# Kernel tuning notes

Measured on AMD Instinct MI355X. Metric: run time of the kernel, lower is better.

Reference implementation:

```python
import jax, jax.numpy as jnp
import numpy as np

CUTOFF = 5.0
MASK_VALUE = -1
N_POINTS = 1024
MAX_NEIGHBOURS = 128
_CELL = np.diag([20.0, 20.0, 20.0]).astype(np.float32)


def _cell_grid():
    # mirrors get_cell_list: integer image multiples bounding the cutoff sphere
    vol = abs(float(np.dot(_CELL[0], np.cross(_CELL[1], _CELL[2]))))
    maxes = []
    for v in range(3):
        clen = float(np.linalg.norm(np.cross(_CELL[(v + 1) % 3], _CELL[(v + 2) % 3])))
        maxes.append(int(np.ceil(CUTOFF / vol * clen)))
    g = np.array(np.meshgrid(np.arange(-maxes[0], maxes[0] + 1),
                             np.arange(-maxes[1], maxes[1] + 1),
                             np.arange(-maxes[2], maxes[2] + 1)))
    reshaped = g.T.reshape(-1, 3)  # (G, 3) integer cell shifts, G = 27 here
    return reshaped.astype(np.int32), reshaped.astype(np.float32) @ _CELL


def setup_inputs() -> dict:
    key = jax.random.key(0)
    cell_list, grid_points = _cell_grid()
    positions = jax.random.uniform(key, (N_POINTS, 3), dtype=jnp.float32, minval=0.0, maxval=20.0)
    return {
        'positions': positions,
        'grid_points': jnp.asarray(grid_points),
        'cell_list': jnp.asarray(cell_list),
        'max_neighbours': MAX_NEIGHBOURS,
    }


def reference(positions, grid_points, cell_list, max_neighbours):
    # Faithful translation of PeriodicBoundary.get_neighbours (include_self=False, include_images=True)
    n = positions.shape[0]
    # all periodic image copies of every point: (G*n, 3)
    neighbours = (grid_points[:, None, :] + positions[None, :, :]).reshape(-1, 3)
    # squared distances from every centre to every image point: (n, G*n)
    d2 = jnp.sum((neighbours[None, :, :] - positions[:, None, :]) ** 2, axis=-1)
    neigh_mask = d2 < CUTOFF * CUTOFF
    # exclude self-interaction (index j == i within the home cell block)
    self_mask = jnp.arange(neighbours.shape[0])[None, :] == jnp.arange(n, dtype=jnp.int32)[:, None]
    neigh_mask = neigh_mask & ~self_mask
    # per-row argwhere compaction into fixed-size padded neighbour lists
    to_idx = jax.vmap(lambda m: jnp.argwhere(m, size=max_neighbours, fill_value=MASK_VALUE))(neigh_mask)[..., 0]
    # cell shift for each flat image index: cells[j] = cell_list[j // n]
    cells = jnp.repeat(cell_list, n, axis=0)  # (G*n, 3)
    cell_indices = jax.vmap(jnp.take, (None, 0, None))(cells, to_idx, 0)  # (n, M, 3)
    neigh = jnp.where(to_idx == MASK_VALUE, MASK_VALUE, to_idx % n)  # (n, M)
    actual_max = jnp.max(neigh_mask.sum(axis=1))
    return neigh, cell_indices, actual_max
```

## Files before the change

kernel.cpp:

```cpp
#include <hip/hip_runtime.h>


#define NPTS 1024
#define MAXN 128
#define CUT2 25.0f
#define NTHR 512
#define NWAVE (NTHR / 64)
#define MAXCHUNK (NPTS / 64)

template <int NC>
__global__ __launch_bounds__(NTHR) void pb_fused(
    const float* __restrict__ positions,
    const float* __restrict__ grid_points,
    const int*   __restrict__ cell_list,
    int n, int G_rt,
    int* __restrict__ neigh,
    int* __restrict__ cells_out,
    int* __restrict__ actual_max)
{
    const int G = (NC > 0) ? NC : G_rt;
    const int nchunk = (n + 63) >> 6;

    __shared__ float4 sp[NPTS];
    __shared__ float4 sgrid[32];
    __shared__ int    scell[32][3];
    __shared__ unsigned long long smask[32][MAXCHUNK];
    __shared__ int    s_choff[32][MAXCHUNK];
    __shared__ int    s_cnt[32];
    __shared__ int    s_coff[32];
    __shared__ int    s_total;

    const int tid = threadIdx.x;

    {
        float* spf = (float*)sp;
        const int n3 = n * 3;
        for (int j = tid; j < n3; j += NTHR) {
            const int p = j / 3, c = j - 3 * p;
            spf[4 * p + c] = positions[j];
        }
        if (tid < G) {
            sgrid[tid] = make_float4(grid_points[3 * tid + 0],
                                     grid_points[3 * tid + 1],
                                     grid_points[3 * tid + 2], 0.0f);
            scell[tid][0] = cell_list[3 * tid + 0];
            scell[tid][1] = cell_list[3 * tid + 1];
            scell[tid][2] = cell_list[3 * tid + 2];
        }
        unsigned long long* smf = (unsigned long long*)smask;
        for (int t = tid; t < G * MAXCHUNK; t += NTHR) smf[t] = 0ull;
    }
    __syncthreads();

    const int i    = blockIdx.x;
    const int wid  = tid >> 6;
    const int lane = tid & 63;

    const float4 ci = sp[i];
    const float cx = ci.x, cy = ci.y, cz = ci.z;

    unsigned long long svmask;
    {
        const float4 g4 = sgrid[lane < G ? lane : 0];
        bool sv = false;
        if (lane < G) {
            const float bx = fmaxf(fmaxf(g4.x - cx, cx - (g4.x + 20.0f)), 0.0f);
            const float by = fmaxf(fmaxf(g4.y - cy, cy - (g4.y + 20.0f)), 0.0f);
            const float bz = fmaxf(fmaxf(g4.z - cz, cz - (g4.z + 20.0f)), 0.0f);
            sv = (bx * bx + by * by + bz * bz < CUT2 + 1.0e-3f);
        }
        svmask = __ballot(sv);
    }

    for (unsigned long long m = svmask; m; m &= m - 1ull) {
        const int c = (int)__builtin_ctzll(m);
        const float4 g4 = sgrid[c];
        for (int ch = wid; ch < nchunk; ch += NWAVE) {
            const int p = (ch << 6) + lane;
            const float4 q = sp[p < n ? p : 0];
            float d2;
            {
#pragma clang fp contract(off)
                const float ex = (g4.x + q.x) - cx;
                const float ey = (g4.y + q.y) - cy;
                const float ez = (g4.z + q.z) - cz;
                d2 = (ex * ex + ey * ey) + ez * ez;
            }
            const bool pred = (p < n) && (d2 < CUT2) && (c * n + p != i);
            const unsigned long long mm = __ballot(pred);
            if (lane == 0) smask[c][ch] = mm;
        }
    }
    __syncthreads();

    if (tid < G * MAXCHUNK) {
        const int c = tid >> 4, ch = tid & 15;
        const int cnt = (ch < nchunk) ? (int)__popcll(smask[c][ch]) : 0;
        int inc = cnt;
#pragma unroll
        for (int d = 1; d < 16; d <<= 1) {
            const int v = __shfl_up(inc, d, 16);
            if ((lane & 15) >= d) inc += v;
        }
        s_choff[c][ch] = inc - cnt;
        if (ch == 15) s_cnt[c] = inc;
    }
    __syncthreads();

    if (wid == 0) {
        const int x = (lane < G) ? s_cnt[lane] : 0;
        int inc = x;
#pragma unroll
        for (int d = 1; d < 32; d <<= 1) {
            const int v = __shfl_up(inc, d, 64);
            if (lane >= d) inc += v;
        }
        if (lane < G) s_coff[lane] = inc - x;
        if (lane == G - 1) s_total = inc;
    }
    __syncthreads();

    int* __restrict__ nrow = neigh + (size_t)i * MAXN;
    int* __restrict__ crow = cells_out + (size_t)i * MAXN * 3;

    {
        const unsigned long long lmask = (1ull << lane) - 1ull;
        for (unsigned long long m = svmask; m; m &= m - 1ull) {
            const int c = (int)__builtin_ctzll(m);
            const int offc = s_coff[c];
            if (offc >= MAXN) continue;
            const int c0 = scell[c][0], c1 = scell[c][1], c2 = scell[c][2];
            for (int ch = wid; ch < nchunk; ch += NWAVE) {
                const unsigned long long mm = smask[c][ch];
                if (!mm) continue;
                const int base2 = offc + s_choff[c][ch];
                if (base2 >= MAXN) continue;
                const int before = __popcll(mm & lmask);
                const int idx = base2 + before;
                if (((mm >> lane) & 1ull) && idx < MAXN) {
                    nrow[idx] = (ch << 6) + lane;
                    crow[3 * idx + 0] = c0;
                    crow[3 * idx + 1] = c1;
                    crow[3 * idx + 2] = c2;
                }
            }
        }
    }

    const int total = s_total;
    const int f0 = scell[G - 1][0], f1 = scell[G - 1][1], f2 = scell[G - 1][2];
    const int base = total < MAXN ? total : MAXN;
    for (int kk = base + tid; kk < MAXN; kk += NTHR) {
        nrow[kk] = -1;
        crow[3 * kk + 0] = f0;
        crow[3 * kk + 1] = f1;
        crow[3 * kk + 2] = f2;
    }

    if (tid == 0) atomicMax(actual_max, total);
}

extern "C" void kernel_launch(void* const* d_in, const int* in_sizes, int n_in,
                              void* d_out, int out_size, void* d_ws, size_t ws_size,
                              hipStream_t stream) {
    const float* positions   = (const float*)d_in[0];
    const float* grid_points = (const float*)d_in[1];
    const int*   cell_list   = (const int*)d_in[2];

    const int n = in_sizes[0] / 3;
    const int G = in_sizes[1] / 3;

    int* out        = (int*)d_out;
    int* neigh      = out;
    int* cells_out  = out + (size_t)n * MAXN;
    int* actual_max = out + (size_t)n * MAXN * 4;

    if (G == 27 && G * MAXCHUNK <= NTHR)
        pb_fused<27><<<n, NTHR, 0, stream>>>(positions, grid_points, cell_list,
                                             n, G, neigh, cells_out, actual_max);
    else
        pb_fused<0><<<n, NTHR, 0, stream>>>(positions, grid_points, cell_list,
                                            n, G, neigh, cells_out, actual_max);
}
```

Measured before the change: 21.02 us.

## Stage neighbour rows in LDS and write out with coalesced int4 stores

Each block now writes its compacted neighbour indices, cell shifts and padding into a shared-memory row buffer, then copies that buffer to global memory with contiguous 16-byte stores from the first 128 threads. This replaces scattered 4-byte global writes whose addresses follow the per-chunk compaction order. The position load into shared memory is also changed to read float4 vectors before de-interleaving. The cost is an extra 2 KB of LDS and one more block-wide barrier before the output copy.

```diff
diff --git a/kernel.cpp b/kernel.cpp
--- a/kernel.cpp
+++ b/kernel.cpp
@@ -29,13 +29,30 @@
     __shared__ int    s_cnt[32];
     __shared__ int    s_coff[32];
     __shared__ int    s_total;
+    __shared__ int4   srow4[MAXN];
+
+    int* srow = (int*)srow4;
 
     const int tid = threadIdx.x;
 
     {
         float* spf = (float*)sp;
         const int n3 = n * 3;
-        for (int j = tid; j < n3; j += NTHR) {
+        const int n4 = n3 >> 2;
+        const float4* pos4 = (const float4*)positions;
+        for (int t = tid; t < n4; t += NTHR) {
+            const float4 f = pos4[t];
+            const int j = 4 * t;
+            const int j0 = j,     p0 = j0 / 3, c0 = j0 - 3 * p0;
+            const int j1 = j + 1, p1 = j1 / 3, c1 = j1 - 3 * p1;
+            const int j2 = j + 2, p2 = j2 / 3, c2 = j2 - 3 * p2;
+            const int j3 = j + 3, p3 = j3 / 3, c3 = j3 - 3 * p3;
+            spf[4 * p0 + c0] = f.x;
+            spf[4 * p1 + c1] = f.y;
+            spf[4 * p2 + c2] = f.z;
+            spf[4 * p3 + c3] = f.w;
+        }
+        for (int j = (n4 << 2) + tid; j < n3; j += NTHR) {
             const int p = j / 3, c = j - 3 * p;
             spf[4 * p + c] = positions[j];
         }
@@ -120,9 +137,6 @@
     }
     __syncthreads();
 
-    int* __restrict__ nrow = neigh + (size_t)i * MAXN;
-    int* __restrict__ crow = cells_out + (size_t)i * MAXN * 3;
-
     {
         const unsigned long long lmask = (1ull << lane) - 1ull;
         for (unsigned long long m = svmask; m; m &= m - 1ull) {
@@ -138,23 +152,33 @@
                 const int before = __popcll(mm & lmask);
                 const int idx = base2 + before;
                 if (((mm >> lane) & 1ull) && idx < MAXN) {
-                    nrow[idx] = (ch << 6) + lane;
-                    crow[3 * idx + 0] = c0;
-                    crow[3 * idx + 1] = c1;
-                    crow[3 * idx + 2] = c2;
+                    srow[idx] = (ch << 6) + lane;
+                    srow[MAXN + 3 * idx + 0] = c0;
+                    srow[MAXN + 3 * idx + 1] = c1;
+                    srow[MAXN + 3 * idx + 2] = c2;
                 }
             }
         }
     }
 
     const int total = s_total;
-    const int f0 = scell[G - 1][0], f1 = scell[G - 1][1], f2 = scell[G - 1][2];
-    const int base = total < MAXN ? total : MAXN;
-    for (int kk = base + tid; kk < MAXN; kk += NTHR) {
-        nrow[kk] = -1;
-        crow[3 * kk + 0] = f0;
-        crow[3 * kk + 1] = f1;
-        crow[3 * kk + 2] = f2;
+    {
+        const int f0 = scell[G - 1][0], f1 = scell[G - 1][1], f2 = scell[G - 1][2];
+        const int base = total < MAXN ? total : MAXN;
+        for (int kk = base + tid; kk < MAXN; kk += NTHR) {
+            srow[kk] = -1;
+            srow[MAXN + 3 * kk + 0] = f0;
+            srow[MAXN + 3 * kk + 1] = f1;
+            srow[MAXN + 3 * kk + 2] = f2;
+        }
+    }
+    __syncthreads();
+
+    {
+        int4* __restrict__ nrow4 = (int4*)(neigh + (size_t)i * MAXN);
+        int4* __restrict__ crow4 = (int4*)(cells_out + (size_t)i * MAXN * 3);
+        if (tid < 32)        nrow4[tid]      = srow4[tid];
+        else if (tid < 128)  crow4[tid - 32] = srow4[tid];
     }
 
     if (tid == 0) atomicMax(actual_max, total);
```

Result: no change. 21.13 us (+0.6%).
